# Optimization experiments

Hardware: AMD Instinct MI355X
Metric: run time of the kernel (lower is better)

The kernel has to match this reference:

```python
import jax, jax.numpy as jnp
import numpy as np

N_NODES = 131072
N_EDGES = 4194304
NUM_GRAPHS = 128


def setup_inputs() -> dict:
    key = jax.random.key(0)
    ks = jax.random.split(key, 12)
    x = jax.random.normal(ks[0], (N_NODES, 3), dtype=jnp.float32)
    edge_index = jax.random.randint(ks[1], (2, N_EDGES), 0, N_NODES, dtype=jnp.int32)
    batch = jnp.sort(jax.random.randint(ks[2], (N_NODES,), 0, NUM_GRAPHS, dtype=jnp.int32))
    W1 = jax.random.normal(ks[3], (3, 16), dtype=jnp.float32) * 0.5
    b1 = jax.random.normal(ks[4], (16,), dtype=jnp.float32) * 0.1
    W2 = jax.random.normal(ks[5], (16, 64), dtype=jnp.float32) * 0.25
    b2 = jax.random.normal(ks[6], (64,), dtype=jnp.float32) * 0.1
    fcw1 = jax.random.normal(ks[7], (64, 32), dtype=jnp.float32) * 0.125
    fcb1 = jax.random.normal(ks[8], (32,), dtype=jnp.float32) * 0.1
    fcw2 = jax.random.normal(ks[9], (32, 2), dtype=jnp.float32) * 0.2
    fcb2 = jax.random.normal(ks[10], (2,), dtype=jnp.float32) * 0.1
    return dict(x=x, edge_index=edge_index, batch=batch, W1=W1, b1=b1,
                W2=W2, b2=b2, fcw1=fcw1, fcb1=fcb1, fcw2=fcw2, fcb2=fcb2)


def _gcn_conv(x, W, b, src, dst, n_nodes):
    # PyG GCNConv: add self-loops, symmetric D^-1/2 A_hat D^-1/2, then scatter-add at dst.
    h = x @ W  # [N, out]
    deg = jax.ops.segment_sum(jnp.ones_like(dst, dtype=h.dtype), dst, num_segments=n_nodes)
    dinv = jnp.where(deg > 0, jax.lax.rsqrt(jnp.maximum(deg, 1.0)), 0.0)
    norm = dinv[src] * dinv[dst]  # [E]
    msgs = norm[:, None] * h[src]  # gather + scale, [E, out]
    return jax.ops.segment_sum(msgs, dst, num_segments=n_nodes) + b


def reference(x, edge_index, batch, W1, b1, W2, b2, fcw1, fcb1, fcw2, fcb2):
    n = x.shape[0]
    loop = jnp.arange(n, dtype=edge_index.dtype)
    src = jnp.concatenate([edge_index[0], loop])
    dst = jnp.concatenate([edge_index[1], loop])
    h = jax.nn.relu(_gcn_conv(x, W1, b1, src, dst, n))
    h = jax.nn.relu(_gcn_conv(h, W2, b2, src, dst, n))
    # global_mean_pool over batch ids
    s = jax.ops.segment_sum(h, batch, num_segments=NUM_GRAPHS)
    cnt = jax.ops.segment_sum(jnp.ones((n,), h.dtype), batch, num_segments=NUM_GRAPHS)
    g = s / jnp.maximum(cnt, 1.0)[:, None]  # [G, 64]
    g = g @ fcw1 + fcb1
    return g @ fcw2 + fcb2  # [G, 2]
```

## Files before the change

### kernel.cpp

```cpp
#include <hip/hip_runtime.h>
#include <hip/hip_fp16.h>

#define N_NODES 131072
#define N_EDGES 4194304
#define NUM_GRAPHS 128

#define NB 512
#define NPB 256
#define BSHIFT 8
#define BCAP 10240
#define GSPAN 8

__global__ __launch_bounds__(512) void k_init(int* __restrict__ bcursor) {
  bcursor[threadIdx.x] = threadIdx.x * BCAP;
}

__global__ __launch_bounds__(1024) void k_binfill(const int* __restrict__ src,
                                                  const int* __restrict__ dst,
                                                  int* __restrict__ bcursor,
                                                  unsigned* __restrict__ binned) {
  __shared__ int hist[NB], base_[NB], rank_[NB];
  for (int k = threadIdx.x; k < NB; k += 1024) { hist[k] = 0; rank_[k] = 0; }
  __syncthreads();
  unsigned pk[16];
  int bk[16];
  int eb = blockIdx.x * 16384 + threadIdx.x;
  #pragma unroll
  for (int i = 0; i < 16; ++i) {
    int e = eb + i * 1024;
    int s = __builtin_nontemporal_load(&src[e]);
    int d = __builtin_nontemporal_load(&dst[e]);
    bk[i] = d >> BSHIFT;
    pk[i] = ((unsigned)s << BSHIFT) | (unsigned)(d & (NPB - 1));
    atomicAdd(&hist[bk[i]], 1);
  }
  __syncthreads();
  for (int k = threadIdx.x; k < NB; k += 1024)
    base_[k] = atomicAdd(&bcursor[k], hist[k]);
  __syncthreads();
  #pragma unroll
  for (int i = 0; i < 16; ++i) {
    int r = atomicAdd(&rank_[bk[i]], 1);
    binned[base_[bk[i]] + r] = pk[i];
  }
}

__global__ __launch_bounds__(1024) void k_sortB(const unsigned* __restrict__ binned,
                                                const int* __restrict__ bcursor,
                                                const float* __restrict__ x,
                                                float* __restrict__ dinv,
                                                float4* __restrict__ xs4,
                                                int* __restrict__ node_off,
                                                int* __restrict__ cnt,
                                                int* __restrict__ csrg) {
  __shared__ int dcount[NPB];
  __shared__ int cursor[NPB];
  __shared__ int wsum[4];
  __shared__ int csrL[BCAP];
  int tid = threadIdx.x;
  if (tid < NPB) dcount[tid] = 0;
  __syncthreads();
  int b = blockIdx.x;
  int s0 = b * BCAP;
  int n = bcursor[b] - s0;

  unsigned ent_r[10];
  #pragma unroll
  for (int j = 0; j < 10; ++j) {
    int e = tid + j * 1024;
    if (e < n) {
      unsigned ent = __builtin_nontemporal_load(&binned[s0 + e]);
      ent_r[j] = ent;
      atomicAdd(&dcount[ent & (NPB - 1)], 1);
    }
  }
  __syncthreads();

  int v = 0, incl = 0;
  if (tid < NPB) {
    v = dcount[tid];
    incl = v;
    #pragma unroll
    for (int d = 1; d < 64; d <<= 1) {
      int t = __shfl_up(incl, d);
      if ((tid & 63) >= d) incl += t;
    }
    if ((tid & 63) == 63) wsum[tid >> 6] = incl;
  }
  __syncthreads();
  if (tid < NPB) {
    int base = 0;
    int wv = tid >> 6;
    for (int w2 = 0; w2 < wv; ++w2) base += wsum[w2];
    int pref = base + incl - v;
    cursor[tid] = pref;
    int node = b * NPB + tid;
    node_off[node] = pref;
    cnt[node] = v;
    float di = rsqrtf((float)(v + 1));
    dinv[node] = di;
    xs4[node] = make_float4(di * x[node * 3 + 0], di * x[node * 3 + 1],
                            di * x[node * 3 + 2], 0.f);
  }
  __syncthreads();

  #pragma unroll
  for (int j = 0; j < 10; ++j) {
    int e = tid + j * 1024;
    if (e < n) {
      unsigned ent = ent_r[j];
      int pos = atomicAdd(&cursor[ent & (NPB - 1)], 1);
      csrL[pos] = (int)(ent >> BSHIFT);
    }
  }
  __syncthreads();

  #pragma unroll
  for (int j = 0; j < 10; ++j) {
    int e = tid + j * 1024;
    if (e < n) csrg[s0 + e] = csrL[e];
  }
}

__global__ __launch_bounds__(1024) void k_agg3h1(const int* __restrict__ csrg,
                                                 const int* __restrict__ bcursor,
                                                 const int* __restrict__ node_off,
                                                 const int* __restrict__ cnt,
                                                 const float* __restrict__ xs,
                                                 const float4* __restrict__ xs4,
                                                 const float* __restrict__ dinv,
                                                 const float* __restrict__ W1,
                                                 const float* __restrict__ b1,
                                                 unsigned* __restrict__ h1h) {
  __shared__ int csrL[BCAP];
  __shared__ float w[48];
  __shared__ float bb[16];
  __shared__ float accS[NPB * 4];
  if (threadIdx.x < 48) w[threadIdx.x] = W1[threadIdx.x];
  if (threadIdx.x >= 64 && threadIdx.x < 80) bb[threadIdx.x - 64] = b1[threadIdx.x - 64];

  int b = blockIdx.x;
  int s0 = b * BCAP;
  int n = bcursor[b] - s0;
  for (int e = threadIdx.x; e < n; e += 1024)
    csrL[e] = __builtin_nontemporal_load(&csrg[s0 + e]);
  __syncthreads();

  int dl = threadIdx.x >> 2;
  int q = threadIdx.x & 3;
  int node = b * NPB + dl;
  int off = node_off[node];
  int len = cnt[node];
  float acc = 0.f;
  #pragma unroll 8
  for (int k = 0; k < len; ++k) {
    int srcn = csrL[off + k];
    acc += xs[srcn * 4 + q];
  }
  accS[threadIdx.x] = acc;
  __syncthreads();

  float di = dinv[node];
  float4 xself = xs4[node];
  float a0 = di * (accS[dl * 4 + 0] + xself.x);
  float a1 = di * (accS[dl * 4 + 1] + xself.y);
  float a2 = di * (accS[dl * 4 + 2] + xself.z);
  float o[4];
  #pragma unroll
  for (int j = 0; j < 4; ++j) {
    int cc = q * 4 + j;
    float vv = a0 * w[cc] + a1 * w[16 + cc] + a2 * w[32 + cc] + bb[cc];
    o[j] = di * fmaxf(vv, 0.f);
  }
  __half2 p0 = __floats2half2_rn(o[0], o[1]);
  __half2 p1 = __floats2half2_rn(o[2], o[3]);
  uint2 st;
  st.x = *reinterpret_cast<unsigned*>(&p0);
  st.y = *reinterpret_cast<unsigned*>(&p1);
  *(uint2*)(h1h + (size_t)node * 8 + q * 2) = st;
}

__global__ __launch_bounds__(1024) void k_agg16pool(const int* __restrict__ csrg,
                                                    const int* __restrict__ bcursor,
                                                    const int* __restrict__ node_off,
                                                    const int* __restrict__ cnt,
                                                    const unsigned* __restrict__ h1h,
                                                    const float* __restrict__ dinv,
                                                    const int* __restrict__ batch,
                                                    const float* __restrict__ W2,
                                                    const float* __restrict__ b2,
                                                    float* __restrict__ gsum) {
  __shared__ int csrL[BCAP];
  __shared__ float aggS[NPB * 16];
  __shared__ float w2s[1024];
  __shared__ float b2s[64];
  __shared__ float gacc[GSPAN * 64];
  w2s[threadIdx.x] = W2[threadIdx.x];
  if (threadIdx.x < 64) b2s[threadIdx.x] = b2[threadIdx.x];
  if (threadIdx.x < GSPAN * 64) gacc[threadIdx.x] = 0.f;

  int b = blockIdx.x;
  int s0 = b * BCAP;
  int n = bcursor[b] - s0;
  for (int e = threadIdx.x; e < n; e += 1024)
    csrL[e] = __builtin_nontemporal_load(&csrg[s0 + e]);
  __syncthreads();

  int q = threadIdx.x & 7;
  int nl0 = threadIdx.x >> 3;
  #pragma unroll
  for (int half = 0; half < 2; ++half) {
    int dl = nl0 + half * 128;
    int node = b * NPB + dl;
    int off = node_off[node];
    int len = cnt[node];
    float o0 = 0.f, o1 = 0.f;
    #pragma unroll 8
    for (int k = 0; k < len; ++k) {
      int srcn = csrL[off + k];
      unsigned hv = h1h[(size_t)srcn * 8 + q];
      __half2 p = *reinterpret_cast<const __half2*>(&hv);
      o0 += __low2float(p);
      o1 += __high2float(p);
    }
    float di = dinv[node];
    unsigned sv = h1h[(size_t)node * 8 + q];
    __half2 sh = *reinterpret_cast<const __half2*>(&sv);
    aggS[dl * 16 + 2 * q + 0] = di * (o0 + __low2float(sh));
    aggS[dl * 16 + 2 * q + 1] = di * (o1 + __high2float(sh));
  }
  __syncthreads();

  int c = threadIdx.x & 63;
  int slot = threadIdx.x >> 6;
  int g0 = batch[b * NPB];
  float racc = 0.f;
  int curli = -1;
  for (int nloc = slot; nloc < NPB; nloc += 16) {
    int nd = b * NPB + nloc;
    int li = batch[nd] - g0;
    if (li != curli) {
      if (curli >= 0) {
        if (curli < GSPAN) atomicAdd(&gacc[curli * 64 + c], racc);
        else atomicAdd(&gsum[(size_t)(g0 + curli) * 64 + c], racc);
      }
      curli = li;
      racc = 0.f;
    }
    float v = b2s[c];
    const float* ar = &aggS[nloc * 16];
    #pragma unroll
    for (int k = 0; k < 16; ++k) v += ar[k] * w2s[k * 64 + c];
    racc += fmaxf(v, 0.f);
  }
  if (curli >= 0) {
    if (curli < GSPAN) atomicAdd(&gacc[curli * 64 + c], racc);
    else atomicAdd(&gsum[(size_t)(g0 + curli) * 64 + c], racc);
  }
  __syncthreads();

  int span = batch[b * NPB + NPB - 1] - g0 + 1;
  if (span > GSPAN) span = GSPAN;
  for (int li = threadIdx.x >> 6; li < span; li += 16) {
    float v = gacc[li * 64 + c];
    atomicAdd(&gsum[(size_t)(g0 + li) * 64 + c], v);
  }
}

__global__ __launch_bounds__(64) void k_fc(const float* __restrict__ gsum,
                                           const int* __restrict__ batch,
                                           const float* __restrict__ fcw1,
                                           const float* __restrict__ fcb1,
                                           const float* __restrict__ fcw2,
                                           const float* __restrict__ fcb2,
                                           float* __restrict__ out) {
  int g = blockIdx.x;
  int lo = 0, hi = N_NODES;
  while (lo < hi) { int m = (lo + hi) >> 1; if (batch[m] < g) lo = m + 1; else hi = m; }
  int start = lo;
  lo = start; hi = N_NODES;
  while (lo < hi) { int m = (lo + hi) >> 1; if (batch[m] < g + 1) lo = m + 1; else hi = m; }
  float inv = 1.0f / fmaxf((float)(lo - start), 1.0f);

  __shared__ float gmean[64];
  gmean[threadIdx.x] = gsum[(size_t)g * 64 + threadIdx.x] * inv;
  __syncthreads();

  __shared__ float hid[32];
  if (threadIdx.x < 32) {
    float a = fcb1[threadIdx.x];
    #pragma unroll
    for (int k = 0; k < 64; ++k) a += gmean[k] * fcw1[k * 32 + threadIdx.x];
    hid[threadIdx.x] = a;
  }
  __syncthreads();

  if (threadIdx.x < 2) {
    float a = fcb2[threadIdx.x];
    #pragma unroll
    for (int k = 0; k < 32; ++k) a += hid[k] * fcw2[k * 2 + threadIdx.x];
    out[g * 2 + threadIdx.x] = a;
  }
}

extern "C" void kernel_launch(void* const* d_in, const int* in_sizes, int n_in,
                              void* d_out, int out_size, void* d_ws, size_t ws_size,
                              hipStream_t stream) {
  const float* x    = (const float*)d_in[0];
  const int*   ei   = (const int*)d_in[1];
  const int*   batch= (const int*)d_in[2];
  const float* W1   = (const float*)d_in[3];
  const float* b1   = (const float*)d_in[4];
  const float* W2   = (const float*)d_in[5];
  const float* b2   = (const float*)d_in[6];
  const float* fcw1 = (const float*)d_in[7];
  const float* fcb1 = (const float*)d_in[8];
  const float* fcw2 = (const float*)d_in[9];
  const float* fcb2 = (const float*)d_in[10];
  float* out = (float*)d_out;

  char* w = (char*)d_ws;
  size_t off = 0;
  auto alloc = [&](size_t bytes) {
    void* p = w + off;
    off += (bytes + 255) & ~(size_t)255;
    return p;
  };
  int*      bcursor  = (int*)     alloc((size_t)NB * 4);
  unsigned* binned   = (unsigned*)alloc((size_t)NB * BCAP * 4);
  int*      csrg     = (int*)     alloc((size_t)NB * BCAP * 4);
  float*    dinv     = (float*)   alloc((size_t)N_NODES * 4);
  float4*   xs4      = (float4*)  alloc((size_t)N_NODES * 16);
  int*      node_off = (int*)     alloc((size_t)N_NODES * 4);
  int*      cnt      = (int*)     alloc((size_t)N_NODES * 4);
  unsigned* h1h      = (unsigned*)alloc((size_t)N_NODES * 32);
  float*    gsum     = (float*)   alloc((size_t)NUM_GRAPHS * 64 * 4);

  const int* srcp = ei;
  const int* dstp = ei + N_EDGES;

  hipMemsetAsync(gsum, 0, (size_t)NUM_GRAPHS * 64 * 4, stream);
  k_init<<<1, 512, 0, stream>>>(bcursor);
  k_binfill<<<N_EDGES / 16384, 1024, 0, stream>>>(srcp, dstp, bcursor, binned);
  k_sortB<<<NB, 1024, 0, stream>>>(binned, bcursor, x, dinv, xs4, node_off, cnt, csrg);
  k_agg3h1<<<NB, 1024, 0, stream>>>(csrg, bcursor, node_off, cnt, (const float*)xs4, xs4, dinv, W1, b1, h1h);
  k_agg16pool<<<NB, 1024, 0, stream>>>(csrg, bcursor, node_off, cnt, h1h, dinv, batch, W2, b2, gsum);
  k_fc<<<NUM_GRAPHS, 64, 0, stream>>>(gsum, batch, fcw1, fcb1, fcw2, fcb2, out);
}
```

Before: 126.8 us.

## Fuse per-bin CSR sort into both aggregation kernels, drop global CSR buffer

Removes the global CSR (csrg, node_off, cnt) write and re-read. Each aggregation kernel now re-sorts its bin's binned entries in shared memory, storing pre-scaled byte offsets. A light k_prep kernel computes only degrees, dinv and the scaled x. The binfill load is also widened to 128-bit vector loads. The trade is that the shared-memory counting sort now runs twice, plus the degree count a third time, in exchange for less global traffic.

```diff
diff --git a/kernel.cpp b/kernel.cpp
--- a/kernel.cpp
+++ b/kernel.cpp
@@ -11,12 +11,14 @@
 #define BCAP 10240
 #define GSPAN 8
 
+typedef int iv4 __attribute__((ext_vector_type(4)));
+
 __global__ __launch_bounds__(512) void k_init(int* __restrict__ bcursor) {
   bcursor[threadIdx.x] = threadIdx.x * BCAP;
 }
 
-__global__ __launch_bounds__(1024) void k_binfill(const int* __restrict__ src,
-                                                  const int* __restrict__ dst,
+__global__ __launch_bounds__(1024) void k_binfill(const iv4* __restrict__ src4,
+                                                  const iv4* __restrict__ dst4,
                                                   int* __restrict__ bcursor,
                                                   unsigned* __restrict__ binned) {
   __shared__ int hist[NB], base_[NB], rank_[NB];
@@ -24,15 +26,19 @@
   __syncthreads();
   unsigned pk[16];
   int bk[16];
-  int eb = blockIdx.x * 16384 + threadIdx.x;
-  #pragma unroll
-  for (int i = 0; i < 16; ++i) {
-    int e = eb + i * 1024;
-    int s = __builtin_nontemporal_load(&src[e]);
-    int d = __builtin_nontemporal_load(&dst[e]);
-    bk[i] = d >> BSHIFT;
-    pk[i] = ((unsigned)s << BSHIFT) | (unsigned)(d & (NPB - 1));
-    atomicAdd(&hist[bk[i]], 1);
+  int q0 = blockIdx.x * 4096 + threadIdx.x;
+  #pragma unroll
+  for (int i = 0; i < 4; ++i) {
+    iv4 sv = __builtin_nontemporal_load(&src4[q0 + i * 1024]);
+    iv4 dv = __builtin_nontemporal_load(&dst4[q0 + i * 1024]);
+    #pragma unroll
+    for (int j = 0; j < 4; ++j) {
+      int idx = i * 4 + j;
+      int s = sv[j], d = dv[j];
+      bk[idx] = d >> BSHIFT;
+      pk[idx] = ((unsigned)s << BSHIFT) | (unsigned)(d & (NPB - 1));
+      atomicAdd(&hist[bk[idx]], 1);
+    }
   }
   __syncthreads();
   for (int k = threadIdx.x; k < NB; k += 1024)
@@ -45,25 +51,55 @@
   }
 }
 
-__global__ __launch_bounds__(1024) void k_sortB(const unsigned* __restrict__ binned,
-                                                const int* __restrict__ bcursor,
-                                                const float* __restrict__ x,
-                                                float* __restrict__ dinv,
-                                                float4* __restrict__ xs4,
-                                                int* __restrict__ node_off,
-                                                int* __restrict__ cnt,
-                                                int* __restrict__ csrg) {
+__global__ __launch_bounds__(1024) void k_prep(const unsigned* __restrict__ binned,
+                                               const int* __restrict__ bcursor,
+                                               const float* __restrict__ x,
+                                               float* __restrict__ dinv,
+                                               float4* __restrict__ xs4) {
   __shared__ int dcount[NPB];
-  __shared__ int cursor[NPB];
-  __shared__ int wsum[4];
-  __shared__ int csrL[BCAP];
   int tid = threadIdx.x;
   if (tid < NPB) dcount[tid] = 0;
   __syncthreads();
   int b = blockIdx.x;
   int s0 = b * BCAP;
   int n = bcursor[b] - s0;
-
+  for (int e = tid; e < n; e += 1024) {
+    unsigned ent = __builtin_nontemporal_load(&binned[s0 + e]);
+    atomicAdd(&dcount[ent & (NPB - 1)], 1);
+  }
+  __syncthreads();
+  if (tid < NPB) {
+    int node = b * NPB + tid;
+    float di = rsqrtf((float)(dcount[tid] + 1));
+    dinv[node] = di;
+    xs4[node] = make_float4(di * x[node * 3 + 0], di * x[node * 3 + 1],
+                            di * x[node * 3 + 2], 0.f);
+  }
+}
+
+__global__ __launch_bounds__(1024) void k_sagg3h1(const unsigned* __restrict__ binned,
+                                                  const int* __restrict__ bcursor,
+                                                  const float* __restrict__ xs,
+                                                  const float4* __restrict__ xs4,
+                                                  const float* __restrict__ dinv,
+                                                  const float* __restrict__ W1,
+                                                  const float* __restrict__ b1,
+                                                  unsigned* __restrict__ h1h) {
+  __shared__ int dcount[NPB], cursor[NPB], nbase[NPB];
+  __shared__ int wsum[4];
+  __shared__ int csrL[BCAP];
+  __shared__ float w[48];
+  __shared__ float bb[16];
+  __shared__ float accS[NPB * 4];
+  int tid = threadIdx.x;
+  if (tid >= 256 && tid < 304) w[tid - 256] = W1[tid - 256];
+  if (tid >= 320 && tid < 336) bb[tid - 320] = b1[tid - 320];
+  if (tid < NPB) dcount[tid] = 0;
+  __syncthreads();
+
+  int b = blockIdx.x;
+  int s0 = b * BCAP;
+  int n = bcursor[b] - s0;
   unsigned ent_r[10];
   #pragma unroll
   for (int j = 0; j < 10; ++j) {
@@ -94,13 +130,7 @@
     for (int w2 = 0; w2 < wv; ++w2) base += wsum[w2];
     int pref = base + incl - v;
     cursor[tid] = pref;
-    int node = b * NPB + tid;
-    node_off[node] = pref;
-    cnt[node] = v;
-    float di = rsqrtf((float)(v + 1));
-    dinv[node] = di;
-    xs4[node] = make_float4(di * x[node * 3 + 0], di * x[node * 3 + 1],
-                            di * x[node * 3 + 2], 0.f);
+    nbase[tid] = pref;
   }
   __syncthreads();
 
@@ -110,54 +140,25 @@
     if (e < n) {
       unsigned ent = ent_r[j];
       int pos = atomicAdd(&cursor[ent & (NPB - 1)], 1);
-      csrL[pos] = (int)(ent >> BSHIFT);
-    }
-  }
-  __syncthreads();
-
-  #pragma unroll
-  for (int j = 0; j < 10; ++j) {
-    int e = tid + j * 1024;
-    if (e < n) csrg[s0 + e] = csrL[e];
-  }
-}
-
-__global__ __launch_bounds__(1024) void k_agg3h1(const int* __restrict__ csrg,
-                                                 const int* __restrict__ bcursor,
-                                                 const int* __restrict__ node_off,
-                                                 const int* __restrict__ cnt,
-                                                 const float* __restrict__ xs,
-                                                 const float4* __restrict__ xs4,
-                                                 const float* __restrict__ dinv,
-                                                 const float* __restrict__ W1,
-                                                 const float* __restrict__ b1,
-                                                 unsigned* __restrict__ h1h) {
-  __shared__ int csrL[BCAP];
-  __shared__ float w[48];
-  __shared__ float bb[16];
-  __shared__ float accS[NPB * 4];
-  if (threadIdx.x < 48) w[threadIdx.x] = W1[threadIdx.x];
-  if (threadIdx.x >= 64 && threadIdx.x < 80) bb[threadIdx.x - 64] = b1[threadIdx.x - 64];
-
-  int b = blockIdx.x;
-  int s0 = b * BCAP;
-  int n = bcursor[b] - s0;
-  for (int e = threadIdx.x; e < n; e += 1024)
-    csrL[e] = __builtin_nontemporal_load(&csrg[s0 + e]);
-  __syncthreads();
-
-  int dl = threadIdx.x >> 2;
-  int q = threadIdx.x & 3;
+      csrL[pos] = (int)(ent >> BSHIFT) << 4;
+    }
+  }
+  __syncthreads();
+
+  int dl = tid >> 2;
+  int q = tid & 3;
   int node = b * NPB + dl;
-  int off = node_off[node];
-  int len = cnt[node];
+  int off = nbase[dl];
+  int len = dcount[dl];
+  const char* xsc = (const char*)xs;
+  int qb = q << 2;
   float acc = 0.f;
   #pragma unroll 8
   for (int k = 0; k < len; ++k) {
-    int srcn = csrL[off + k];
-    acc += xs[srcn * 4 + q];
-  }
-  accS[threadIdx.x] = acc;
+    int bo = csrL[off + k];
+    acc += *(const float*)(xsc + bo + qb);
+  }
+  accS[tid] = acc;
   __syncthreads();
 
   float di = dinv[node];
@@ -180,45 +181,91 @@
   *(uint2*)(h1h + (size_t)node * 8 + q * 2) = st;
 }
 
-__global__ __launch_bounds__(1024) void k_agg16pool(const int* __restrict__ csrg,
-                                                    const int* __restrict__ bcursor,
-                                                    const int* __restrict__ node_off,
-                                                    const int* __restrict__ cnt,
-                                                    const unsigned* __restrict__ h1h,
-                                                    const float* __restrict__ dinv,
-                                                    const int* __restrict__ batch,
-                                                    const float* __restrict__ W2,
-                                                    const float* __restrict__ b2,
-                                                    float* __restrict__ gsum) {
+__global__ __launch_bounds__(1024) void k_sagg16pool(const unsigned* __restrict__ binned,
+                                                     const int* __restrict__ bcursor,
+                                                     const unsigned* __restrict__ h1h,
+                                                     const float* __restrict__ dinv,
+                                                     const int* __restrict__ batch,
+                                                     const float* __restrict__ W2,
+                                                     const float* __restrict__ b2,
+                                                     float* __restrict__ gsum) {
+  __shared__ int dcount[NPB], cursor[NPB], nbase[NPB];
+  __shared__ int wsum[4];
   __shared__ int csrL[BCAP];
   __shared__ float aggS[NPB * 16];
   __shared__ float w2s[1024];
   __shared__ float b2s[64];
   __shared__ float gacc[GSPAN * 64];
-  w2s[threadIdx.x] = W2[threadIdx.x];
-  if (threadIdx.x < 64) b2s[threadIdx.x] = b2[threadIdx.x];
-  if (threadIdx.x < GSPAN * 64) gacc[threadIdx.x] = 0.f;
+  int tid = threadIdx.x;
+  w2s[tid] = W2[tid];
+  if (tid < 64) b2s[tid] = b2[tid];
+  if (tid < GSPAN * 64) gacc[tid] = 0.f;
+  if (tid < NPB) dcount[tid] = 0;
+  __syncthreads();
 
   int b = blockIdx.x;
   int s0 = b * BCAP;
   int n = bcursor[b] - s0;
-  for (int e = threadIdx.x; e < n; e += 1024)
-    csrL[e] = __builtin_nontemporal_load(&csrg[s0 + e]);
-  __syncthreads();
-
-  int q = threadIdx.x & 7;
-  int nl0 = threadIdx.x >> 3;
+  unsigned ent_r[10];
+  #pragma unroll
+  for (int j = 0; j < 10; ++j) {
+    int e = tid + j * 1024;
+    if (e < n) {
+      unsigned ent = __builtin_nontemporal_load(&binned[s0 + e]);
+      ent_r[j] = ent;
+      atomicAdd(&dcount[ent & (NPB - 1)], 1);
+    }
+  }
+  __syncthreads();
+
+  int v = 0, incl = 0;
+  if (tid < NPB) {
+    v = dcount[tid];
+    incl = v;
+    #pragma unroll
+    for (int d = 1; d < 64; d <<= 1) {
+      int t = __shfl_up(incl, d);
+      if ((tid & 63) >= d) incl += t;
+    }
+    if ((tid & 63) == 63) wsum[tid >> 6] = incl;
+  }
+  __syncthreads();
+  if (tid < NPB) {
+    int base = 0;
+    int wv = tid >> 6;
+    for (int w2 = 0; w2 < wv; ++w2) base += wsum[w2];
+    int pref = base + incl - v;
+    cursor[tid] = pref;
+    nbase[tid] = pref;
+  }
+  __syncthreads();
+
+  #pragma unroll
+  for (int j = 0; j < 10; ++j) {
+    int e = tid + j * 1024;
+    if (e < n) {
+      unsigned ent = ent_r[j];
+      int pos = atomicAdd(&cursor[ent & (NPB - 1)], 1);
+      csrL[pos] = (int)(ent >> BSHIFT) << 5;
+    }
+  }
+  __syncthreads();
+
+  const char* h1c = (const char*)h1h;
+  int q = tid & 7;
+  int qb = q << 2;
+  int nl0 = tid >> 3;
   #pragma unroll
   for (int half = 0; half < 2; ++half) {
     int dl = nl0 + half * 128;
     int node = b * NPB + dl;
-    int off = node_off[node];
-    int len = cnt[node];
+    int off = nbase[dl];
+    int len = dcount[dl];
     float o0 = 0.f, o1 = 0.f;
     #pragma unroll 8
     for (int k = 0; k < len; ++k) {
-      int srcn = csrL[off + k];
-      unsigned hv = h1h[(size_t)srcn * 8 + q];
+      int bo = csrL[off + k];
+      unsigned hv = *(const unsigned*)(h1c + bo + qb);
       __half2 p = *reinterpret_cast<const __half2*>(&hv);
       o0 += __low2float(p);
       o1 += __high2float(p);
@@ -231,8 +278,8 @@
   }
   __syncthreads();
 
-  int c = threadIdx.x & 63;
-  int slot = threadIdx.x >> 6;
+  int c = tid & 63;
+  int slot = tid >> 6;
   int g0 = batch[b * NPB];
   float racc = 0.f;
   int curli = -1;
@@ -247,11 +294,11 @@
       curli = li;
       racc = 0.f;
     }
-    float v = b2s[c];
+    float vv = b2s[c];
     const float* ar = &aggS[nloc * 16];
     #pragma unroll
-    for (int k = 0; k < 16; ++k) v += ar[k] * w2s[k * 64 + c];
-    racc += fmaxf(v, 0.f);
+    for (int k = 0; k < 16; ++k) vv += ar[k] * w2s[k * 64 + c];
+    racc += fmaxf(vv, 0.f);
   }
   if (curli >= 0) {
     if (curli < GSPAN) atomicAdd(&gacc[curli * 64 + c], racc);
@@ -261,9 +308,8 @@
 
   int span = batch[b * NPB + NPB - 1] - g0 + 1;
   if (span > GSPAN) span = GSPAN;
-  for (int li = threadIdx.x >> 6; li < span; li += 16) {
-    float v = gacc[li * 64 + c];
-    atomicAdd(&gsum[(size_t)(g0 + li) * 64 + c], v);
+  for (int li = tid >> 6; li < span; li += 16) {
+    atomicAdd(&gsum[(size_t)(g0 + li) * 64 + c], gacc[li * 64 + c]);
   }
 }
 
@@ -326,24 +372,21 @@
     off += (bytes + 255) & ~(size_t)255;
     return p;
   };
-  int*      bcursor  = (int*)     alloc((size_t)NB * 4);
-  unsigned* binned   = (unsigned*)alloc((size_t)NB * BCAP * 4);
-  int*      csrg     = (int*)     alloc((size_t)NB * BCAP * 4);
-  float*    dinv     = (float*)   alloc((size_t)N_NODES * 4);
-  float4*   xs4      = (float4*)  alloc((size_t)N_NODES * 16);
-  int*      node_off = (int*)     alloc((size_t)N_NODES * 4);
-  int*      cnt      = (int*)     alloc((size_t)N_NODES * 4);
-  unsigned* h1h      = (unsigned*)alloc((size_t)N_NODES * 32);
-  float*    gsum     = (float*)   alloc((size_t)NUM_GRAPHS * 64 * 4);
-
-  const int* srcp = ei;
-  const int* dstp = ei + N_EDGES;
+  int*      bcursor = (int*)     alloc((size_t)NB * 4);
+  unsigned* binned  = (unsigned*)alloc((size_t)NB * BCAP * 4);
+  float*    dinv    = (float*)   alloc((size_t)N_NODES * 4);
+  float4*   xs4     = (float4*)  alloc((size_t)N_NODES * 16);
+  unsigned* h1h     = (unsigned*)alloc((size_t)N_NODES * 32);
+  float*    gsum    = (float*)   alloc((size_t)NUM_GRAPHS * 64 * 4);
+
+  const iv4* src4 = (const iv4*)ei;
+  const iv4* dst4 = (const iv4*)(ei + N_EDGES);
 
   hipMemsetAsync(gsum, 0, (size_t)NUM_GRAPHS * 64 * 4, stream);
   k_init<<<1, 512, 0, stream>>>(bcursor);
-  k_binfill<<<N_EDGES / 16384, 1024, 0, stream>>>(srcp, dstp, bcursor, binned);
-  k_sortB<<<NB, 1024, 0, stream>>>(binned, bcursor, x, dinv, xs4, node_off, cnt, csrg);
-  k_agg3h1<<<NB, 1024, 0, stream>>>(csrg, bcursor, node_off, cnt, (const float*)xs4, xs4, dinv, W1, b1, h1h);
-  k_agg16pool<<<NB, 1024, 0, stream>>>(csrg, bcursor, node_off, cnt, h1h, dinv, batch, W2, b2, gsum);
+  k_binfill<<<N_EDGES / 16384, 1024, 0, stream>>>(src4, dst4, bcursor, binned);
+  k_prep<<<NB, 1024, 0, stream>>>(binned, bcursor, x, dinv, xs4);
+  k_sagg3h1<<<NB, 1024, 0, stream>>>(binned, bcursor, (const float*)xs4, xs4, dinv, W1, b1, h1h);
+  k_sagg16pool<<<NB, 1024, 0, stream>>>(binned, bcursor, h1h, dinv, batch, W2, b2, gsum);
   k_fc<<<NUM_GRAPHS, 64, 0, stream>>>(gsum, batch, fcw1, fcb1, fcw2, fcb2, out);
 }
```

Result: faster. 120.0 us (-5.3%).
